# Kernel tuning notes

Measured on AMD Instinct MI355X. Metric: run time of the kernel, lower is better.

## Reference

```python
import jax, jax.numpy as jnp
import numpy as np

ALPHA = 0.25
GAMMA = 2.0
W_CLASS = W_BBOX = W_GIOU = W_MASK = W_DICE = W_PROJ = 1.0
EPS = 1e-8


def box_cxcywh_to_xyxy(b):
    cx, cy, w, h = jnp.split(b, 4, axis=-1)
    return jnp.concatenate([cx - 0.5 * w, cy - 0.5 * h, cx + 0.5 * w, cy + 0.5 * h], axis=-1)


def dice_coef(inputs, targets):
    # inputs: logits [N, D]; targets: binary [M, D]
    s = jax.nn.sigmoid(inputs)
    num = 2.0 * jnp.einsum('nd,md->nm', s, targets)
    den = s.sum(-1)[:, None] + targets.sum(-1)[None, :]
    return (num + 1.0) / (den + 1.0)  # [N, M]


def sigmoid_focal_coef(inputs, targets):
    # inputs: logits [N, D]; targets: binary [M, D] -> [N, M]
    x = inputs[:, None, :]
    t = targets[None, :, :]
    p = jax.nn.sigmoid(x)
    # BCE-with-logits, numerically stable
    ce = jnp.maximum(x, 0.0) - x * t + jnp.log1p(jnp.exp(-jnp.abs(x)))
    p_t = p * t + (1.0 - p) * (1.0 - t)
    alpha_t = ALPHA * t + (1.0 - ALPHA) * (1.0 - t)
    return (alpha_t * ce * (1.0 - p_t) ** GAMMA).mean(-1)


def giou_cost(src_xyxy, tgt_xyxy):
    # src [nf, nq, 4], tgt [nf, 1, 4] -> cost [nf, nq, 1]
    a1 = (src_xyxy[..., 2] - src_xyxy[..., 0]) * (src_xyxy[..., 3] - src_xyxy[..., 1])
    a2 = (tgt_xyxy[..., 2] - tgt_xyxy[..., 0]) * (tgt_xyxy[..., 3] - tgt_xyxy[..., 1])
    lt = jnp.maximum(src_xyxy[:, :, None, :2], tgt_xyxy[:, None, :, :2])
    rb = jnp.minimum(src_xyxy[:, :, None, 2:], tgt_xyxy[:, None, :, 2:])
    wh = jnp.clip(rb - lt, 0.0)
    inter = wh[..., 0] * wh[..., 1]
    union = a1[:, :, None] + a2[:, None, :] - inter
    iou = inter / union
    ltc = jnp.minimum(src_xyxy[:, :, None, :2], tgt_xyxy[:, None, :, :2])
    rbc = jnp.maximum(src_xyxy[:, :, None, 2:], tgt_xyxy[:, None, :, 2:])
    whc = jnp.clip(rbc - ltc, 0.0)
    areac = whc[..., 0] * whc[..., 1]
    giou = iou - (areac - union) / areac
    return -giou


def cost_matrix_one(logits, boxes, masks, tmask, tbox, tvalid):
    # logits [nf,nq,1], boxes [nf,nq,4], masks [nf,nq,H,W], tmask [nf,H,W], tbox [nf,4], tvalid [nf]
    p = jax.nn.sigmoid(logits[..., 0])  # [nf, nq]
    neg = (1.0 - ALPHA) * p ** GAMMA * (-jnp.log(1.0 - p + EPS))
    pos = ALPHA * (1.0 - p) ** GAMMA * (-jnp.log(p + EPS))
    w = (tvalid != 0).astype(p.dtype)  # valid-frame mask replaces python `continue`
    cost_class = (((pos - neg) * w[:, None]).sum(0) / w.sum())[:, None]  # [nq, 1]

    cost_bbox = jnp.abs(boxes[:, :, None, :] - tbox[:, None, None, :]).sum(-1).mean(0)  # [nq, 1]
    cost_giou = giou_cost(box_cxcywh_to_xyxy(boxes), box_cxcywh_to_xyxy(tbox[:, None, :])).mean(0)

    out_mask = jnp.transpose(masks, (1, 0, 2, 3))  # [nq, nf, H, W]
    nq = out_mask.shape[0]
    flat_src = out_mask.reshape(nq, -1)
    flat_tgt = tmask.reshape(1, -1)
    cost_mask = sigmoid_focal_coef(flat_src, flat_tgt)  # [nq, 1]
    cost_dice = -dice_coef(flat_src, flat_tgt)

    src_y = jnp.max(out_mask, axis=2, keepdims=True).reshape(nq, -1)  # [nq, nf*W]
    src_x = jnp.max(out_mask, axis=3, keepdims=True).reshape(nq, -1)  # [nq, nf*H]
    tgt_y = jnp.max(tmask[None], axis=2, keepdims=True).reshape(1, -1)
    tgt_x = jnp.max(tmask[None], axis=3, keepdims=True).reshape(1, -1)
    cost_proj = -0.5 * (dice_coef(src_y, tgt_y) + dice_coef(src_x, tgt_x))

    C = (W_CLASS * cost_class + W_BBOX * cost_bbox + W_GIOU * cost_giou
         + W_MASK * cost_mask + W_DICE * cost_dice + W_PROJ * cost_proj)
    return C  # [nq, 1]


def setup_inputs() -> dict:
    key = jax.random.key(0)
    k = jax.random.split(key, 6)
    bs, nf, nq, H, W = 2, 8, 300, 96, 96
    pred_logits = jax.random.normal(k[0], (bs, nf, nq, 1), dtype=jnp.float32)
    pred_boxes = jax.random.uniform(k[1], (bs, nf, nq, 4), dtype=jnp.float32)
    pred_masks = jax.random.normal(k[2], (bs, nf, nq, H, W), dtype=jnp.float32)
    target_masks = (jax.random.uniform(k[3], (bs, nf, H, W)) < 0.3).astype(jnp.float32)
    tgt_boxes = jax.random.uniform(k[4], (bs, nf, 4), dtype=jnp.float32)
    tgt_valid = jnp.ones((bs, nf), dtype=jnp.int32)
    valid_pad = jnp.zeros((bs, H, W), dtype=bool)
    return {"pred_logits": pred_logits, "pred_boxes": pred_boxes, "pred_masks": pred_masks,
            "target_masks": target_masks, "tgt_boxes": tgt_boxes, "tgt_valid": tgt_valid,
            "valid_pad": valid_pad}


def reference(pred_logits, pred_boxes, pred_masks, target_masks, tgt_boxes, tgt_valid, valid_pad):
    # zero out predictions over padded regions (masked_fill with valid[:, None, None])
    masks = jnp.where(valid_pad[:, None, None, :, :], 0.0, pred_masks)
    C = jax.vmap(cost_matrix_one)(pred_logits, pred_boxes, masks, target_masks, tgt_boxes, tgt_valid)
    src_ind = jnp.argmin(C, axis=1).astype(jnp.int64)  # [bs, 1]
    tgt_ind = jnp.zeros_like(src_ind)
    return C, src_ind, tgt_ind
```

## Files before the change

### kernel.cpp

```cpp
#include <hip/hip_runtime.h>
#include <math.h>

#define NF 8
#define NQ 300
#define HSZ 96
#define WSZ 96
#define HW (HSZ*WSZ)
#define DTOT (NF*HW)
#define NBF 16

#define WS_TGTY  0
#define WS_TGTX  1536
#define WS_TSUM  3072
#define WS_YSUM  3088
#define WS_XSUM  3104
#define WS_TBITS 3136
#define WS_PBITS 7744
#define WS_PART  8320

__device__ __forceinline__ float sigmoid_fast(float x) {
    float e = __expf(-fabsf(x));
    float inv = __builtin_amdgcn_rcpf(1.f + e);
    return x >= 0.f ? inv : e * inv;
}

#define NTT 1024
__global__ __launch_bounds__(NTT)
void targets_kernel(const float* __restrict__ tm, const unsigned char* __restrict__ vpad,
                    float* __restrict__ ws) {
    int bf = blockIdx.x, t = threadIdx.x;
    int lane = t & 63, wid = t >> 6;
    __shared__ float tile[HSZ * 97];
    __shared__ float redt[16 * 3];
    const float* base = tm + (size_t)bf * HW;
    unsigned* tbw = (unsigned*)(ws + WS_TBITS) + bf * 288;

    float tsum = 0.f;
    #pragma unroll
    for (int it = 0; it < 9; ++it) {
        int e = it * NTT + t;
        float v = base[e];
        tsum += v;
        tile[e + e / 96] = v;
        unsigned long long m = __ballot(v != 0.f);
        int word = it * 32 + wid * 2;
        if (lane == 0)       tbw[word]     = (unsigned)m;
        else if (lane == 32) tbw[word + 1] = (unsigned)(m >> 32);
    }
    if ((bf & 7) == 0) {
        const unsigned char* vb = vpad + (size_t)(bf >> 3) * HW;
        unsigned* pbw = (unsigned*)(ws + WS_PBITS) + (bf >> 3) * 288;
        #pragma unroll
        for (int it = 0; it < 9; ++it) {
            int e = it * NTT + t;
            unsigned long long m = __ballot(vb[e] != 0);
            int word = it * 32 + wid * 2;
            if (lane == 0)       pbw[word]     = (unsigned)m;
            else if (lane == 32) pbw[word + 1] = (unsigned)(m >> 32);
        }
    }
    __syncthreads();

    float ysum = 0.f, xsum = 0.f;
    if (t < 96) {
        float m = -INFINITY;
        #pragma unroll 8
        for (int h = 0; h < HSZ; ++h) m = fmaxf(m, tile[h * 97 + t]);
        ws[WS_TGTY + bf * 96 + t] = m;
        ysum = m;
    } else if (t < 192) {
        int hh = t - 96;
        float m = -INFINITY;
        #pragma unroll 8
        for (int w = 0; w < WSZ; ++w) m = fmaxf(m, tile[hh * 97 + w]);
        ws[WS_TGTX + bf * 96 + hh] = m;
        xsum = m;
    }
    float s0 = tsum, s1 = ysum, s2 = xsum;
    #pragma unroll
    for (int off = 32; off > 0; off >>= 1) {
        s0 += __shfl_down(s0, off, 64);
        s1 += __shfl_down(s1, off, 64);
        s2 += __shfl_down(s2, off, 64);
    }
    if (lane == 0) { redt[wid * 3] = s0; redt[wid * 3 + 1] = s1; redt[wid * 3 + 2] = s2; }
    __syncthreads();
    if (t == 0) {
        float a0 = 0.f, a1 = 0.f, a2 = 0.f;
        #pragma unroll
        for (int w = 0; w < 16; ++w) {
            a0 += redt[w * 3]; a1 += redt[w * 3 + 1]; a2 += redt[w * 3 + 2];
        }
        ws[WS_TSUM + bf] = a0;
        ws[WS_YSUM + bf] = a1;
        ws[WS_XSUM + bf] = a2;
    }
}

#define NTP 384
#define QPB 4
__global__ __launch_bounds__(NTP, 4)
void partial_kernel(const float* __restrict__ masks, const float* __restrict__ ws,
                    float* __restrict__ part) {
    int bid = blockIdx.x;
    int bf  = bid / (NQ / QPB);
    int q0  = (bid - bf * (NQ / QPB)) * QPB;
    int b   = bf >> 3, f = bf & 7;
    int t   = threadIdx.x;
    int w4  = t % 24;
    int r0  = t / 24;
    int wsh = (t & 7) * 4;

    __shared__ float rp[96 * 25];
    __shared__ float cp[16 * 100];
    __shared__ float red[6][8];

    const unsigned* tbw = (const unsigned*)(ws + WS_TBITS) + bf * 288;
    const unsigned* pbw = (const unsigned*)(ws + WS_PBITS) + b * 288;

    unsigned tw[6], pw[6];
    #pragma unroll
    for (int k = 0; k < 6; ++k) tw[k] = tbw[k * 48 + (t >> 3)];
    #pragma unroll
    for (int k = 0; k < 6; ++k) pw[k] = pbw[k * 48 + (t >> 3)];
    float gy = 0.f, gx = 0.f;
    if (t < 96)       gy = ws[WS_TGTY + bf * 96 + t];
    else if (t < 192) gx = ws[WS_TGTX + bf * 96 + (t - 96)];

    const float4* mrow = (const float4*)(masks + (size_t)(bf * NQ + q0) * HW);

    float4 xa[6], xb[6];
    #pragma unroll
    for (int k = 0; k < 6; ++k) xa[k] = mrow[k * NTP + t];

    #pragma unroll
    for (int i = 0; i < QPB; ++i) {
        if (i + 1 < QPB) {
            const float4* mnext = mrow + (size_t)(i + 1) * (HW / 4);
            #pragma unroll
            for (int k = 0; k < 6; ++k) xb[k] = mnext[k * NTP + t];
        }

        float focal = 0.f, dnum = 0.f, dden = 0.f;
        float cm0 = -INFINITY, cm1 = -INFINITY, cm2 = -INFINITY, cm3 = -INFINITY;

        #pragma unroll
        for (int k = 0; k < 6; ++k) {
            unsigned tn = (tw[k] >> wsh) & 0xFu;
            unsigned pn = (pw[k] >> wsh) & 0xFu;
            float xs[4] = {xa[k].x, xa[k].y, xa[k].z, xa[k].w};
            if (pn) {
                #pragma unroll
                for (int j = 0; j < 4; ++j) if ((pn >> j) & 1u) xs[j] = 0.f;
            }
            float rmx = -INFINITY;
            #pragma unroll
            for (int j = 0; j < 4; ++j) {
                float x = xs[j];
                float tg = (float)((tn >> j) & 1u);
                float e = __expf(-fabsf(x));
                float se = 1.f + e;
                float inv = __builtin_amdgcn_rcpf(se);
                float s = x >= 0.f ? inv : e * inv;
                float L = __logf(se);
                float ce = fmaf(-x, tg, fmaxf(x, 0.f) + L);
                float omp = fmaf(tg, fmaf(-2.f, s, 1.f), s);
                float at = fmaf(tg, -0.5f, 0.75f);
                focal = fmaf(at * ce, omp * omp, focal);
                dnum = fmaf(s, tg, dnum);
                dden += s;
                rmx = fmaxf(rmx, x);
            }
            cm0 = fmaxf(cm0, xs[0]); cm1 = fmaxf(cm1, xs[1]);
            cm2 = fmaxf(cm2, xs[2]); cm3 = fmaxf(cm3, xs[3]);
            rp[(16 * k + r0) * 25 + w4] = rmx;
        }
        {
            float4 cmv = {cm0, cm1, cm2, cm3};
            *(float4*)&cp[r0 * 100 + w4 * 4] = cmv;
        }
        asm volatile("s_waitcnt lgkmcnt(0)" ::: "memory");
        __builtin_amdgcn_s_barrier();

        float v0 = focal, v1 = dnum, v2 = dden, v3 = 0.f, v4 = 0.f, v5 = 0.f, v6 = 0.f;
        if (t < 96) {
            float m = -INFINITY;
            #pragma unroll
            for (int p = 0; p < 16; ++p) m = fmaxf(m, cp[p * 100 + t]);
            float sg = sigmoid_fast(m);
            v4 = sg;
            v3 = sg * gy;
        } else if (t < 192) {
            int r = t - 96;
            float m = rp[r * 25];
            #pragma unroll
            for (int c = 1; c < 24; ++c) m = fmaxf(m, rp[r * 25 + c]);
            float sg = sigmoid_fast(m);
            v6 = sg;
            v5 = sg * gx;
        }
        #pragma unroll
        for (int off = 32; off > 0; off >>= 1) {
            v0 += __shfl_down(v0, off, 64);
            v1 += __shfl_down(v1, off, 64);
            v2 += __shfl_down(v2, off, 64);
            v3 += __shfl_down(v3, off, 64);
            v4 += __shfl_down(v4, off, 64);
            v5 += __shfl_down(v5, off, 64);
            v6 += __shfl_down(v6, off, 64);
        }
        int wid = t >> 6, lane = t & 63;
        if (lane == 0) {
            red[wid][0] = v0; red[wid][1] = v1; red[wid][2] = v2; red[wid][3] = v3;
            red[wid][4] = v4; red[wid][5] = v5; red[wid][6] = v6;
        }
        asm volatile("s_waitcnt lgkmcnt(0)" ::: "memory");
        __builtin_amdgcn_s_barrier();
        if (t == 0) {
            float* o = part + (size_t)((b * NQ + q0 + i) * NF + f) * 8;
            #pragma unroll
            for (int ii = 0; ii < 7; ++ii)
                o[ii] = red[0][ii] + red[1][ii] + red[2][ii] + red[3][ii] + red[4][ii] + red[5][ii];
        }

        if (i + 1 < QPB) {
            #pragma unroll
            for (int k = 0; k < 6; ++k) xa[k] = xb[k];
        }
    }
}

#define NTC 64
__global__ __launch_bounds__(NTC)
void combine_kernel(const float* __restrict__ logits, const float* __restrict__ boxes,
                    const float* __restrict__ tbox, const int* __restrict__ tvalid,
                    const float* __restrict__ ws, float* __restrict__ out) {
    int gid = blockIdx.x * NTC + threadIdx.x;
    if (gid >= 2 * NQ) return;
    int b = gid / NQ, q = gid - b * NQ;

    const float* pbase = ws + WS_PART + (size_t)gid * (NF * 8);
    float focal = 0.f, dnum = 0.f, dden = 0.f;
    float pYn = 0.f, pYd = 0.f, pXn = 0.f, pXd = 0.f;
    float tsum = 0.f, ysum = 0.f, xsum = 0.f;
    #pragma unroll
    for (int f = 0; f < NF; ++f) {
        int bf = b * NF + f;
        const float* p = pbase + f * 8;
        focal += p[0]; dnum += p[1]; dden += p[2];
        pYn += p[3]; pYd += p[4]; pXn += p[5]; pXd += p[6];
        tsum += ws[WS_TSUM + bf];
        ysum += ws[WS_YSUM + bf];
        xsum += ws[WS_XSUM + bf];
    }
    float cost_mask = focal / (float)DTOT;
    float cost_dice = -(2.f * dnum + 1.f) / (dden + tsum + 1.f);
    float coefY = (2.f * pYn + 1.f) / (pYd + ysum + 1.f);
    float coefX = (2.f * pXn + 1.f) / (pXd + xsum + 1.f);
    float cost_proj = -0.5f * (coefY + coefX);

    float wsum = 0.f, cls = 0.f, cb = 0.f, cg = 0.f;
    #pragma unroll
    for (int f = 0; f < NF; ++f) {
        float wv = (tvalid[b * NF + f] != 0) ? 1.f : 0.f;
        wsum += wv;
        float lg = logits[(b * NF + f) * NQ + q];
        float p = sigmoid_fast(lg);
        float negc = 0.75f * p * p * (-__logf(1.f - p + 1e-8f));
        float posc = 0.25f * (1.f - p) * (1.f - p) * (-__logf(p + 1e-8f));
        cls += (posc - negc) * wv;

        const float* bx = boxes + (size_t)((b * NF + f) * NQ + q) * 4;
        const float* tb = tbox + (b * NF + f) * 4;
        float cx = bx[0], cy = bx[1], bw = bx[2], bh = bx[3];
        float tcx = tb[0], tcy = tb[1], tbw = tb[2], tbh = tb[3];
        cb += fabsf(cx - tcx) + fabsf(cy - tcy) + fabsf(bw - tbw) + fabsf(bh - tbh);
        float sx1 = cx - 0.5f * bw, sy1 = cy - 0.5f * bh;
        float sx2 = cx + 0.5f * bw, sy2 = cy + 0.5f * bh;
        float tx1 = tcx - 0.5f * tbw, ty1 = tcy - 0.5f * tbh;
        float tx2 = tcx + 0.5f * tbw, ty2 = tcy + 0.5f * tbh;
        float a1 = (sx2 - sx1) * (sy2 - sy1), a2 = (tx2 - tx1) * (ty2 - ty1);
        float iw = fmaxf(fminf(sx2, tx2) - fmaxf(sx1, tx1), 0.f);
        float ih = fmaxf(fminf(sy2, ty2) - fmaxf(sy1, ty1), 0.f);
        float inter = iw * ih;
        float uni = a1 + a2 - inter;
        float iou = inter / uni;
        float cw = fmaxf(fmaxf(sx2, tx2) - fminf(sx1, tx1), 0.f);
        float chh = fmaxf(fmaxf(sy2, ty2) - fminf(sy1, ty1), 0.f);
        float areac = cw * chh;
        cg += -(iou - (areac - uni) / areac);
    }
    cls /= wsum;
    cb *= 0.125f;
    cg *= 0.125f;
    out[b * NQ + q] = cls + cb + cg + cost_mask + cost_dice + cost_proj;
}

#define NT 256
__global__ __launch_bounds__(NT)
void argmin_kernel(float* __restrict__ out, int write_idx) {
    int b = blockIdx.x, t = threadIdx.x;
    float best = INFINITY;
    int bi = 0x7fffffff;
    for (int q = t; q < NQ; q += NT) {
        float v = out[b * NQ + q];
        if (v < best) { best = v; bi = q; }
    }
    #pragma unroll
    for (int off = 32; off > 0; off >>= 1) {
        float ov = __shfl_down(best, off, 64);
        int oi = __shfl_down(bi, off, 64);
        if (ov < best || (ov == best && oi < bi)) { best = ov; bi = oi; }
    }
    __shared__ float rv[4];
    __shared__ int ri[4];
    int wid = t >> 6, lane = t & 63;
    if (lane == 0) { rv[wid] = best; ri[wid] = bi; }
    __syncthreads();
    if (t == 0 && write_idx) {
        #pragma unroll
        for (int w = 1; w < 4; ++w) {
            if (rv[w] < best || (rv[w] == best && ri[w] < bi)) { best = rv[w]; bi = ri[w]; }
        }
        out[2 * NQ + b] = (float)bi;
        out[2 * NQ + 2 + b] = 0.f;
    }
}

extern "C" void kernel_launch(void* const* d_in, const int* in_sizes, int n_in,
                              void* d_out, int out_size, void* d_ws, size_t ws_size,
                              hipStream_t stream) {
    const float* logits = (const float*)d_in[0];
    const float* boxes  = (const float*)d_in[1];
    const float* masks  = (const float*)d_in[2];
    const float* tmask  = (const float*)d_in[3];
    const float* tbox   = (const float*)d_in[4];
    const int*   tvalid = (const int*)d_in[5];
    const unsigned char* vpad = (const unsigned char*)d_in[6];
    float* out = (float*)d_out;
    float* ws  = (float*)d_ws;

    targets_kernel<<<NBF, NTT, 0, stream>>>(tmask, vpad, ws);
    partial_kernel<<<NBF * (NQ / QPB), NTP, 0, stream>>>(masks, ws, ws + WS_PART);
    combine_kernel<<<(2 * NQ + NTC - 1) / NTC, NTC, 0, stream>>>(logits, boxes, tbox,
                                                                 tvalid, ws, out);
    int write_idx = (out_size >= 2 * NQ + 4) ? 1 : 0;
    argmin_kernel<<<2, NT, 0, stream>>>(out, write_idx);
}
```

Before: 349.8 us.

## Stage mask tiles through LDS with async global-to-LDS double buffering

The partial kernel now streams each query's mask in two half-tiles using global_load_lds directly into a double-buffered shared-memory array, instead of prefetching the next query into registers. Each block also handles 2 queries instead of 4, the occupancy hint drops from 4 to 3, and the final partial-sum write is spread over 7 threads. The aim is to cut register pressure and overlap global loads with the transcendental-heavy compute. In exchange it uses much more LDS per block, adds extra barriers and LDS reads, and doubles the number of blocks.

```diff
diff --git a/kernel.cpp b/kernel.cpp
--- a/kernel.cpp
+++ b/kernel.cpp
@@ -23,6 +23,11 @@
     float inv = __builtin_amdgcn_rcpf(1.f + e);
     return x >= 0.f ? inv : e * inv;
 }
+
+#define GLD_LDS16(gsrc, ldst) \
+    __builtin_amdgcn_global_load_lds( \
+        (const __attribute__((address_space(1))) void*)(const void*)(gsrc), \
+        (__attribute__((address_space(3))) void*)(void*)(ldst), 16, 0, 0)
 
 #define NTT 1024
 __global__ __launch_bounds__(NTT)
@@ -98,8 +103,10 @@
 }
 
 #define NTP 384
-#define QPB 4
-__global__ __launch_bounds__(NTP, 4)
+#define QPB 2
+#define HF4 1152
+#define HFL (HF4*4)
+__global__ __launch_bounds__(NTP, 3)
 void partial_kernel(const float* __restrict__ masks, const float* __restrict__ ws,
                     float* __restrict__ part) {
     int bid = blockIdx.x;
@@ -111,6 +118,7 @@
     int r0  = t / 24;
     int wsh = (t & 7) * 4;
 
+    __shared__ float sbuf[2][HFL];
     __shared__ float rp[96 * 25];
     __shared__ float cp[16 * 100];
     __shared__ float red[6][8];
@@ -127,28 +135,39 @@
     if (t < 96)       gy = ws[WS_TGTY + bf * 96 + t];
     else if (t < 192) gx = ws[WS_TGTX + bf * 96 + (t - 96)];
 
-    const float4* mrow = (const float4*)(masks + (size_t)(bf * NQ + q0) * HW);
-
-    float4 xa[6], xb[6];
-    #pragma unroll
-    for (int k = 0; k < 6; ++k) xa[k] = mrow[k * NTP + t];
-
-    #pragma unroll
-    for (int i = 0; i < QPB; ++i) {
-        if (i + 1 < QPB) {
-            const float4* mnext = mrow + (size_t)(i + 1) * (HW / 4);
-            #pragma unroll
-            for (int k = 0; k < 6; ++k) xb[k] = mnext[k * NTP + t];
-        }
-
-        float focal = 0.f, dnum = 0.f, dden = 0.f;
-        float cm0 = -INFINITY, cm1 = -INFINITY, cm2 = -INFINITY, cm3 = -INFINITY;
-
-        #pragma unroll
-        for (int k = 0; k < 6; ++k) {
+    asm volatile("s_waitcnt vmcnt(0)" ::: "memory");
+
+    const float4* mbase = (const float4*)(masks + (size_t)(bf * NQ + q0) * HW);
+
+    #define STAGE(s) do {                                                   \
+        const float4* _src = mbase + (size_t)(s) * HF4 + t;                 \
+        _Pragma("unroll")                                                   \
+        for (int kk = 0; kk < 3; ++kk)                                      \
+            GLD_LDS16(_src + kk * NTP, &sbuf[(s) & 1][(kk * NTP + t) * 4]); \
+    } while (0)
+
+    STAGE(0);
+
+    float focal = 0.f, dnum = 0.f, dden = 0.f;
+    float cm0 = -INFINITY, cm1 = -INFINITY, cm2 = -INFINITY, cm3 = -INFINITY;
+
+    #pragma unroll
+    for (int s = 0; s < 2 * QPB; ++s) {
+        if (s + 1 < 2 * QPB) {
+            STAGE(s + 1);
+            asm volatile("s_waitcnt vmcnt(3)" ::: "memory");
+        } else {
+            asm volatile("s_waitcnt vmcnt(0)" ::: "memory");
+        }
+        __builtin_amdgcn_s_barrier();
+
+        #pragma unroll
+        for (int kk = 0; kk < 3; ++kk) {
+            int k = (s & 1) * 3 + kk;
+            float4 xv = *(const float4*)&sbuf[s & 1][(kk * NTP + t) * 4];
             unsigned tn = (tw[k] >> wsh) & 0xFu;
             unsigned pn = (pw[k] >> wsh) & 0xFu;
-            float xs[4] = {xa[k].x, xa[k].y, xa[k].z, xa[k].w};
+            float xs[4] = {xv.x, xv.y, xv.z, xv.w};
             if (pn) {
                 #pragma unroll
                 for (int j = 0; j < 4; ++j) if ((pn >> j) & 1u) xs[j] = 0.f;
@@ -161,20 +180,26 @@
                 float e = __expf(-fabsf(x));
                 float se = 1.f + e;
                 float inv = __builtin_amdgcn_rcpf(se);
-                float s = x >= 0.f ? inv : e * inv;
+                float s_ = x >= 0.f ? inv : e * inv;
                 float L = __logf(se);
                 float ce = fmaf(-x, tg, fmaxf(x, 0.f) + L);
-                float omp = fmaf(tg, fmaf(-2.f, s, 1.f), s);
+                float omp = fmaf(tg, fmaf(-2.f, s_, 1.f), s_);
                 float at = fmaf(tg, -0.5f, 0.75f);
                 focal = fmaf(at * ce, omp * omp, focal);
-                dnum = fmaf(s, tg, dnum);
-                dden += s;
+                dnum = fmaf(s_, tg, dnum);
+                dden += s_;
                 rmx = fmaxf(rmx, x);
             }
             cm0 = fmaxf(cm0, xs[0]); cm1 = fmaxf(cm1, xs[1]);
             cm2 = fmaxf(cm2, xs[2]); cm3 = fmaxf(cm3, xs[3]);
             rp[(16 * k + r0) * 25 + w4] = rmx;
         }
+
+        if ((s & 1) == 0) {
+            __builtin_amdgcn_s_barrier();
+            continue;
+        }
+
         {
             float4 cmv = {cm0, cm1, cm2, cm3};
             *(float4*)&cp[r0 * 100 + w4 * 4] = cmv;
@@ -216,18 +241,16 @@
         }
         asm volatile("s_waitcnt lgkmcnt(0)" ::: "memory");
         __builtin_amdgcn_s_barrier();
-        if (t == 0) {
-            float* o = part + (size_t)((b * NQ + q0 + i) * NF + f) * 8;
-            #pragma unroll
-            for (int ii = 0; ii < 7; ++ii)
-                o[ii] = red[0][ii] + red[1][ii] + red[2][ii] + red[3][ii] + red[4][ii] + red[5][ii];
-        }
-
-        if (i + 1 < QPB) {
-            #pragma unroll
-            for (int k = 0; k < 6; ++k) xa[k] = xb[k];
-        }
-    }
+        if (t < 7) {
+            float tot = red[0][t] + red[1][t] + red[2][t] + red[3][t] + red[4][t] + red[5][t];
+            part[(size_t)((b * NQ + q0 + (s >> 1)) * NF + f) * 8 + t] = tot;
+        }
+        __builtin_amdgcn_s_barrier();
+
+        focal = 0.f; dnum = 0.f; dden = 0.f;
+        cm0 = -INFINITY; cm1 = -INFINITY; cm2 = -INFINITY; cm3 = -INFINITY;
+    }
+    #undef STAGE
 }
 
 #define NTC 64
```

Measured after the change: 328.1 us. 6.2% less time.
